# Kernel tuning notes

Measured on AMD Instinct MI355X. Metric: run time of the kernel, lower is better.

## Reference

```python
import jax, jax.numpy as jnp
import numpy as np

B, C, N, E = 8, 16, 512, 1024


def setup_inputs() -> dict:
    key = jax.random.key(0)
    k1, k2, k3, k4 = jax.random.split(key, 4)
    adj = jax.random.normal(k1, (B, C, N, N), dtype=jnp.float32)
    mask = jax.random.bernoulli(k2, 0.5, (B, N, N))
    edge_index = jax.random.randint(k3, (B, E, 2), 0, N, dtype=jnp.int32)
    edge_attr = jax.random.randint(k4, (B, E), 0, C, dtype=jnp.int32)
    return {"adj": adj, "mask": mask, "edge_index": edge_index, "edge_attr": edge_attr}


def reference(adj, mask, edge_index, edge_attr):
    # adj: [B, C, N, N] logits; mask: [B, N, N] bool; edge_index: [B, E, 2]; edge_attr: [B, E]
    b, c, n, _ = adj.shape
    e = edge_index.shape[1]
    # Scatter gold edge labels into a [B, N, N] label grid (default class 0).
    b_idx = jnp.broadcast_to(jnp.arange(b, dtype=jnp.int32)[:, None], (b, e))
    ans = jnp.zeros((b, n, n), dtype=jnp.int32).at[
        b_idx, edge_index[:, :, 0], edge_index[:, :, 1]
    ].set(edge_attr)
    # Cross-entropy over class dim; positions with mask == False are ignored (label -100 in torch).
    logp = jax.nn.log_softmax(adj, axis=1)  # [B, C, N, N]
    nll = -jnp.take_along_axis(logp, ans[:, None, :, :], axis=1)[:, 0]  # [B, N, N]
    valid = mask.astype(adj.dtype)
    count = jnp.maximum(jnp.sum(valid, axis=(1, 2)), 1.0)
    per_sample = jnp.sum(nll * valid, axis=(1, 2)) / count  # reduction='mean' per sample
    return jnp.sum(per_sample) / b
```

## Files before the change

### kernel.cpp

```cpp
#include <hip/hip_runtime.h>

#define Bn 8
#define Cn 16
#define Nn 512
#define En 1024
#define QPB 65536
#define HSZ 2048


__global__ __launch_bounds__(256) void main_pass(const float4* __restrict__ adj4,
                                                 const int4* __restrict__ mask4,
                                                 float* __restrict__ ws) {
    const int b   = blockIdx.x >> 8;
    const int off = ((blockIdx.x & 255) << 8) + threadIdx.x;
    const float4* base = adj4 + (size_t)b * (size_t)(Cn * QPB) + off;

    float4 x0;
    float s0 = 0.f, s1 = 0.f, s2 = 0.f, s3 = 0.f;
#pragma unroll
    for (int c = 0; c < Cn; ++c) {
        float4 v = base[c * QPB];
        if (c == 0) x0 = v;
        s0 += __expf(v.x);
        s1 += __expf(v.y);
        s2 += __expf(v.z);
        s3 += __expf(v.w);
    }
    const int4 m = mask4[(size_t)b * QPB + off];

    float S = 0.f, cnt = 0.f;
    if (m.x) { S += __logf(s0) - x0.x; cnt += 1.f; }
    if (m.y) { S += __logf(s1) - x0.y; cnt += 1.f; }
    if (m.z) { S += __logf(s2) - x0.z; cnt += 1.f; }
    if (m.w) { S += __logf(s3) - x0.w; cnt += 1.f; }

#pragma unroll
    for (int d = 32; d; d >>= 1) {
        S   += __shfl_down(S, d, 64);
        cnt += __shfl_down(cnt, d, 64);
    }
    __shared__ float sh[8];
    const int wave = threadIdx.x >> 6;
    const int lane = threadIdx.x & 63;
    if (lane == 0) { sh[wave] = S; sh[4 + wave] = cnt; }
    __syncthreads();
    if (threadIdx.x == 0) {
        float St = sh[0] + sh[1] + sh[2] + sh[3];
        float Ct = sh[4] + sh[5] + sh[6] + sh[7];
        atomicAdd(&ws[b * 4 + 0], St);
        atomicAdd(&ws[b * 4 + 1], Ct);
    }
}

__global__ __launch_bounds__(1024) void edge_pass(const float* __restrict__ adj,
                                                  const int* __restrict__ mask,
                                                  const int* __restrict__ eidx,
                                                  const int* __restrict__ eattr,
                                                  const float* __restrict__ ws,
                                                  float* __restrict__ out) {
    const int b = blockIdx.x;
    const int e = threadIdx.x;

    __shared__ int   keys[HSZ];
    __shared__ int   maxe[HSZ];
    __shared__ float corr;

    keys[e]       = -1;
    keys[e + En]  = -1;
    maxe[e]       = -1;
    maxe[e + En]  = -1;
    if (e == 0) corr = 0.f;

    const int2 rc   = ((const int2*)eidx)[b * En + e];
    const int  attr = eattr[b * En + e];
    const int  key  = (rc.x << 9) | rc.y;
    __syncthreads();

    unsigned h = ((unsigned)key * 2654435761u) >> 21;
    int slot = -1;
    for (;;) {
        int prev = atomicCAS(&keys[h], -1, key);
        if (prev == -1 || prev == key) { slot = (int)h; break; }
        h = (h + 1) & (HSZ - 1);
    }
    atomicMax(&maxe[slot], e);
    __syncthreads();

    float val = 0.f;
    if (maxe[slot] == e && attr != 0 &&
        mask[(size_t)b * Nn * Nn + rc.x * Nn + rc.y] != 0) {
        const size_t p0 = (((size_t)b * Cn) * Nn + rc.x) * Nn + rc.y;
        val = adj[p0] - adj[p0 + (size_t)attr * Nn * Nn];
    }
#pragma unroll
    for (int d = 32; d; d >>= 1) val += __shfl_down(val, d, 64);
    if ((threadIdx.x & 63) == 0 && val != 0.f) atomicAdd(&corr, val);
    __syncthreads();

    if (e == 0) {
        const float cnt = fmaxf(ws[b * 4 + 1], 1.0f);
        const float t = (ws[b * 4 + 0] + corr) / cnt;
        atomicAdd(out, t * (1.0f / (float)Bn));
    }
}

extern "C" void kernel_launch(void* const* d_in, const int* in_sizes, int n_in,
                              void* d_out, int out_size, void* d_ws, size_t ws_size,
                              hipStream_t stream) {
    const float* adj  = (const float*)d_in[0];
    const int*   mask = (const int*)d_in[1];
    const int*   eidx = (const int*)d_in[2];
    const int*   eatt = (const int*)d_in[3];
    float*       out  = (float*)d_out;
    float*       ws   = (float*)d_ws;

    hipMemsetAsync(d_ws, 0, 32 * sizeof(float), stream);
    hipMemsetAsync(d_out, 0, sizeof(float), stream);
    main_pass<<<dim3(Bn * 256), dim3(256), 0, stream>>>(
        (const float4*)adj, (const int4*)mask, ws);
    edge_pass<<<dim3(Bn), dim3(En), 0, stream>>>(adj, mask, eidx, eatt, ws, out);
}
```

Before: 217.0 us.

## Double per-thread work, use nontemporal loads, replace atomics with per-block partials

Each main_pass thread now handles two float4 quads (eight positions), halving the grid to 1024 blocks, and loads adj and mask with nontemporal hints. Per-block sums are written to distinct workspace slots instead of being added atomically, and edge_pass reduces those 128 partials per sample itself. This drops the workspace memset and the global atomic contention. In exchange each thread uses more registers, and with half as many threads there is less parallelism to hide memory latency.

```diff
diff --git a/kernel.cpp b/kernel.cpp
--- a/kernel.cpp
+++ b/kernel.cpp
@@ -6,33 +6,52 @@
 #define En 1024
 #define QPB 65536
 #define HSZ 2048
+#define MBLK 1024
+
+typedef float fx4 __attribute__((ext_vector_type(4)));
+typedef int   ix4 __attribute__((ext_vector_type(4)));
 
 
-__global__ __launch_bounds__(256) void main_pass(const float4* __restrict__ adj4,
-                                                 const int4* __restrict__ mask4,
-                                                 float* __restrict__ ws) {
-    const int b   = blockIdx.x >> 8;
-    const int off = ((blockIdx.x & 255) << 8) + threadIdx.x;
-    const float4* base = adj4 + (size_t)b * (size_t)(Cn * QPB) + off;
+__global__ __launch_bounds__(256, 4) void main_pass(const fx4* __restrict__ adj4,
+                                                    const ix4* __restrict__ mask4,
+                                                    float* __restrict__ ws) {
+    const int bid = blockIdx.x;
+    const int b   = bid >> 7;
+    const int q0  = (((bid & 127) << 8) + threadIdx.x) << 1;
+    const fx4* base = adj4 + (size_t)b * (size_t)(Cn * QPB) + q0;
 
-    float4 x0;
+    fx4 x0a, x0b;
     float s0 = 0.f, s1 = 0.f, s2 = 0.f, s3 = 0.f;
+    float s4 = 0.f, s5 = 0.f, s6 = 0.f, s7 = 0.f;
+
 #pragma unroll
-    for (int c = 0; c < Cn; ++c) {
-        float4 v = base[c * QPB];
-        if (c == 0) x0 = v;
-        s0 += __expf(v.x);
-        s1 += __expf(v.y);
-        s2 += __expf(v.z);
-        s3 += __expf(v.w);
+    for (int c = 0; c < 8; ++c) {
+        fx4 va = __builtin_nontemporal_load(&base[(size_t)c * QPB]);
+        fx4 vb = __builtin_nontemporal_load(&base[(size_t)c * QPB + 1]);
+        if (c == 0) { x0a = va; x0b = vb; }
+        s0 += __expf(va.x); s1 += __expf(va.y); s2 += __expf(va.z); s3 += __expf(va.w);
+        s4 += __expf(vb.x); s5 += __expf(vb.y); s6 += __expf(vb.z); s7 += __expf(vb.w);
     }
-    const int4 m = mask4[(size_t)b * QPB + off];
+#pragma unroll
+    for (int c = 8; c < 16; ++c) {
+        fx4 va = __builtin_nontemporal_load(&base[(size_t)c * QPB]);
+        fx4 vb = __builtin_nontemporal_load(&base[(size_t)c * QPB + 1]);
+        s0 += __expf(va.x); s1 += __expf(va.y); s2 += __expf(va.z); s3 += __expf(va.w);
+        s4 += __expf(vb.x); s5 += __expf(vb.y); s6 += __expf(vb.z); s7 += __expf(vb.w);
+    }
+
+    const ix4 ma = __builtin_nontemporal_load(&mask4[(size_t)b * QPB + q0]);
+    const ix4 mb = __builtin_nontemporal_load(&mask4[(size_t)b * QPB + q0 + 1]);
 
     float S = 0.f, cnt = 0.f;
-    if (m.x) { S += __logf(s0) - x0.x; cnt += 1.f; }
-    if (m.y) { S += __logf(s1) - x0.y; cnt += 1.f; }
-    if (m.z) { S += __logf(s2) - x0.z; cnt += 1.f; }
-    if (m.w) { S += __logf(s3) - x0.w; cnt += 1.f; }
+    if (ma.x) { S += __logf(s0) - x0a.x; cnt += 1.f; }
+    if (ma.y) { S += __logf(s1) - x0a.y; cnt += 1.f; }
+    if (ma.z) { S += __logf(s2) - x0a.z; cnt += 1.f; }
+    if (ma.w) { S += __logf(s3) - x0a.w; cnt += 1.f; }
+    if (mb.x) { S += __logf(s4) - x0b.x; cnt += 1.f; }
+    if (mb.y) { S += __logf(s5) - x0b.y; cnt += 1.f; }
+    if (mb.z) { S += __logf(s6) - x0b.z; cnt += 1.f; }
+    if (mb.w) { S += __logf(s7) - x0b.w; cnt += 1.f; }
 
 #pragma unroll
     for (int d = 32; d; d >>= 1) {
@@ -41,14 +60,11 @@
     }
     __shared__ float sh[8];
     const int wave = threadIdx.x >> 6;
-    const int lane = threadIdx.x & 63;
-    if (lane == 0) { sh[wave] = S; sh[4 + wave] = cnt; }
+    if ((threadIdx.x & 63) == 0) { sh[wave] = S; sh[4 + wave] = cnt; }
     __syncthreads();
     if (threadIdx.x == 0) {
-        float St = sh[0] + sh[1] + sh[2] + sh[3];
-        float Ct = sh[4] + sh[5] + sh[6] + sh[7];
-        atomicAdd(&ws[b * 4 + 0], St);
-        atomicAdd(&ws[b * 4 + 1], Ct);
+        ws[bid * 2 + 0] = sh[0] + sh[1] + sh[2] + sh[3];
+        ws[bid * 2 + 1] = sh[4] + sh[5] + sh[6] + sh[7];
     }
 }
 
@@ -63,17 +79,29 @@
 
     __shared__ int   keys[HSZ];
     __shared__ int   maxe[HSZ];
-    __shared__ float corr;
+    __shared__ float shS[16], shC[16], shV[16];
 
-    keys[e]       = -1;
-    keys[e + En]  = -1;
-    maxe[e]       = -1;
-    maxe[e + En]  = -1;
-    if (e == 0) corr = 0.f;
+    keys[e]      = -1;
+    keys[e + En] = -1;
+    maxe[e]      = -1;
+    maxe[e + En] = -1;
 
+    float Sp = 0.f, Cp = 0.f;
+    if (e < 128) {
+        Sp = ws[(b * 128 + e) * 2 + 0];
+        Cp = ws[(b * 128 + e) * 2 + 1];
+    }
     const int2 rc   = ((const int2*)eidx)[b * En + e];
     const int  attr = eattr[b * En + e];
     const int  key  = (rc.x << 9) | rc.y;
+
+#pragma unroll
+    for (int d = 32; d; d >>= 1) {
+        Sp += __shfl_down(Sp, d, 64);
+        Cp += __shfl_down(Cp, d, 64);
+    }
+    const int wave = e >> 6;
+    if ((e & 63) == 0) { shS[wave] = Sp; shC[wave] = Cp; }
     __syncthreads();
 
     unsigned h = ((unsigned)key * 2654435761u) >> 21;
@@ -94,12 +122,16 @@
     }
 #pragma unroll
     for (int d = 32; d; d >>= 1) val += __shfl_down(val, d, 64);
-    if ((threadIdx.x & 63) == 0 && val != 0.f) atomicAdd(&corr, val);
+    if ((e & 63) == 0) shV[wave] = val;
     __syncthreads();
 
     if (e == 0) {
-        const float cnt = fmaxf(ws[b * 4 + 1], 1.0f);
-        const float t = (ws[b * 4 + 0] + corr) / cnt;
+        float S = shS[0] + shS[1];
+        float C = shC[0] + shC[1];
+        float corr = 0.f;
+#pragma unroll
+        for (int w = 0; w < 16; ++w) corr += shV[w];
+        const float t = (S + corr) / fmaxf(C, 1.0f);
         atomicAdd(out, t * (1.0f / (float)Bn));
     }
 }
@@ -114,9 +146,8 @@
     float*       out  = (float*)d_out;
     float*       ws   = (float*)d_ws;
 
-    hipMemsetAsync(d_ws, 0, 32 * sizeof(float), stream);
-    hipMemsetAsync(d_out, 0, sizeof(float), stream);
-    main_pass<<<dim3(Bn * 256), dim3(256), 0, stream>>>(
-        (const float4*)adj, (const int4*)mask, ws);
+    (void)hipMemsetAsync(d_out, 0, sizeof(float), stream);
+    main_pass<<<dim3(MBLK), dim3(256), 0, stream>>>(
+        (const fx4*)adj, (const ix4*)mask, ws);
     edge_pass<<<dim3(Bn), dim3(En), 0, stream>>>(adj, mask, eidx, eatt, ws, out);
 }
```

Result: faster. 199.0 us (-8.3%).
